# Performance work log

Hardware: AMD Instinct MI355X
Metric: run time of the kernel (lower is better)

## Reference

```python
import jax, jax.numpy as jnp
import numpy as np

B, T, D = 64, 1024, 256   # batch, steps, obs dim
H, L, S = 512, 64, 4      # rnn hidden, latent dim, num_samples
LOG_2PI = float(np.log(2.0 * np.pi))


def setup_inputs() -> dict:
    key = jax.random.key(0)
    ks = jax.random.split(key, 6)
    return {
        "inputs": jax.random.normal(ks[0], (B, T, D), dtype=jnp.float32),
        "noise": jax.random.normal(ks[1], (T, S * B, L), dtype=jnp.float32),
        "W_x": jax.random.normal(ks[2], (D + L, 3 * H), dtype=jnp.float32) * 0.05,
        "W_h": jax.random.normal(ks[3], (H, 3 * H), dtype=jnp.float32) * 0.05,
        "b": jnp.zeros((3 * H,), dtype=jnp.float32),
        "W_d": jax.random.normal(ks[4], (H, 2 * L), dtype=jnp.float32) * 0.05,
        "b_d": jnp.zeros((2 * L,), dtype=jnp.float32),
    }


def _forward(inputs, noise, W_x, W_h, b, W_d, b_d):
    # inputs: [B, T, D]; scan over time with carry (rnn_state h, prev latent z)
    xs_t = jnp.swapaxes(inputs, 0, 1)  # [T, B, D]

    def step(carry, xs):
        h, z_prev = carry              # h: [S*B, H], z_prev: [S*B, L]
        x_t, eps_t = xs                # x_t: [B, D], eps_t: [S*B, L]
        x_tiled = jnp.tile(x_t, (S, 1))            # [S*B, D]
        rnn_in = jnp.concatenate([x_tiled, z_prev], axis=-1)  # [S*B, D+L]
        xg = rnn_in @ W_x + b                      # [S*B, 3H]
        hg_zr = h @ W_h[:, : 2 * H]                # update/reset recurrent part
        z_gate = jax.nn.sigmoid(xg[:, :H] + hg_zr[:, :H])
        r_gate = jax.nn.sigmoid(xg[:, H : 2 * H] + hg_zr[:, H:])
        n_cand = jnp.tanh(xg[:, 2 * H :] + (r_gate * h) @ W_h[:, 2 * H :])
        h_new = (1.0 - z_gate) * n_cand + z_gate * h  # GRU state, rnn_out == h_new
        # posterior dist p(z[t] | h[t]): diag Gaussian
        dp = h_new @ W_d + b_d                     # [S*B, 2L]
        mu, raw = dp[:, :L], dp[:, L:]
        sigma = jax.nn.softplus(raw) + 1e-4
        log_sigma = jnp.log(sigma)
        z = mu + sigma * eps_t                     # reparameterized sample
        ent = jnp.sum(0.5 * (LOG_2PI + 1.0) + log_sigma, axis=-1)          # [S*B]
        lp = jnp.sum(-0.5 * eps_t * eps_t - log_sigma - 0.5 * LOG_2PI, axis=-1)
        return (h_new, z), (z, ent, lp)

    h0 = jnp.zeros((S * B, H), dtype=inputs.dtype)
    z0 = jnp.zeros((S * B, L), dtype=inputs.dtype)
    _, (zs, ents, lps) = jax.lax.scan(step, (h0, z0), (xs_t, noise))
    # zs: [T, S*B, L] -> [S, B, T, L]
    sampled_z = jnp.swapaxes(zs, 0, 1).reshape(S, B, T, L)
    entropies = jnp.swapaxes(ents, 0, 1).reshape(S, B, T)
    log_probs = jnp.swapaxes(lps, 0, 1).reshape(S, B, T)
    return sampled_z, entropies, log_probs


def reference(inputs, noise, W_x, W_h, b, W_d, b_d):
    return _forward(inputs, noise, W_x, W_h, b, W_d, b_d)
```

## Files before the change

kernel.cpp:

```cpp
#include <hip/hip_runtime.h>
#include <stdint.h>


#define NWG  128u

typedef __bf16 bf16;
typedef __attribute__((ext_vector_type(8))) __bf16 bf16x8;
typedef __attribute__((ext_vector_type(8))) short  s16x8;
typedef __attribute__((ext_vector_type(4))) float  f32x4;
typedef __attribute__((ext_vector_type(4))) unsigned int u32x4;
typedef __attribute__((ext_vector_type(2))) unsigned long long u64x2;

__device__ __forceinline__ f32x4 mfma16(bf16x8 a, bf16x8 b, f32x4 c) {
  return __builtin_amdgcn_mfma_f32_16x16x32_bf16(
      __builtin_bit_cast(s16x8, a), __builtin_bit_cast(s16x8, b), c, 0, 0, 0);
}

__global__ void repack_kernel(const float* __restrict__ W_x,
                              const float* __restrict__ W_h,
                              const float* __restrict__ W_d,
                              bf16* __restrict__ Whs, bf16* __restrict__ Wxz,
                              bf16* __restrict__ Wdf, bf16* __restrict__ Wxx)
{
  unsigned e = blockIdx.x*256u + threadIdx.x;
  if (e < 786432u) {
    unsigned c = e/49152u, r0 = e%49152u;
    unsigned kc = r0/3072u, r1 = r0%3072u;
    unsigned q = r1/768u, r2 = r1%768u;
    unsigned n = r2/8u, j = r2%8u;
    unsigned k = kc*32u + q*8u + j;
    unsigned colg = (n>>5)*512u + c*32u + (n&31u);
    Whs[e] = (bf16)W_h[k*1536u + colg];
  } else if (e < 884736u) {
    unsigned e1 = e - 786432u;
    unsigned c = e1/6144u, r0 = e1%6144u;
    unsigned kc = r0/3072u, r1 = r0%3072u;
    unsigned q = r1/768u, r2 = r1%768u;
    unsigned n = r2/8u, j = r2%8u;
    unsigned k = 256u + kc*32u + q*8u + j;
    unsigned colg = (n>>5)*512u + c*32u + (n&31u);
    Wxz[e1] = (bf16)W_x[k*1536u + colg];
  } else if (e < 950272u) {
    unsigned e2 = e - 884736u;
    unsigned kc = e2/4096u, r0 = e2%4096u;
    unsigned q = r0/1024u, r1 = r0%1024u;
    unsigned n = r1/8u, j = r1%8u;
    unsigned k = kc*32u + q*8u + j;
    Wdf[e2] = (bf16)W_d[k*128u + n];
  } else if (e < 1343488u) {
    unsigned e3 = e - 950272u;
    unsigned c = e3/24576u, r0 = e3%24576u;
    unsigned kc = r0/3072u, r1 = r0%3072u;
    unsigned q = r1/768u, r2 = r1%768u;
    unsigned n = r2/8u, j = r2%8u;
    unsigned k = kc*32u + q*8u + j;
    unsigned colg = (n>>5)*512u + c*32u + (n&31u);
    Wxx[e3] = (bf16)W_x[k*1536u + colg];
  }
}

__global__ void xpose_kernel(const float* __restrict__ x, bf16* __restrict__ xT)
{
  unsigned t = blockIdx.x, tid = threadIdx.x;
  unsigned row = tid>>2, seg = tid&3u;
  const float* src = x + ((size_t)row*1024u + t)*256u + seg*64u;
  bf16* dst = xT + (size_t)t*16384u + row*256u + seg*64u;
  #pragma unroll
  for (int i = 0; i < 8; ++i) {
    f32x4 v0 = *(const f32x4*)(src + i*8);
    f32x4 v1 = *(const f32x4*)(src + i*8 + 4);
    bf16x8 o;
    #pragma unroll
    for (int j = 0; j < 4; ++j) { o[j] = (bf16)v0[j]; o[4+j] = (bf16)v1[j]; }
    *(bf16x8*)(dst + i*8) = o;
  }
}

__global__ void __launch_bounds__(256) xgx_kernel(const bf16* __restrict__ xT,
                                                  const bf16* __restrict__ Wxx,
                                                  const float* __restrict__ bias,
                                                  bf16* __restrict__ xgx,
                                                  unsigned t0)
{
  __shared__ bf16 WxS[24576];
  __shared__ bf16 otile[6144];
  unsigned bid = blockIdx.x, lt = bid>>4, c = bid&15u, tid = threadIdx.x;
  unsigned t = t0 + lt;
  { const u32x4* s = (const u32x4*)(Wxx + (size_t)c*24576u); u32x4* d = (u32x4*)WxS;
    #pragma unroll
    for (int i=0;i<12;i++) d[tid+256u*i] = s[tid+256u*i]; }
  __syncthreads();
  unsigned wave = tid>>6, lane = tid&63u, q = lane>>4, m = lane&15u;
  f32x4 zero4 = {0.f,0.f,0.f,0.f};
  f32x4 acc[6];
  #pragma unroll
  for (int nt=0;nt<6;nt++) acc[nt] = zero4;
  const bf16* ap = xT + (size_t)t*16384u + (16u*wave + m)*256u + q*8u;
  #pragma unroll
  for (int kc=0;kc<8;kc++) {
    bf16x8 a = *(const bf16x8*)(ap + kc*32);
    #pragma unroll
    for (int nt=0;nt<6;nt++) {
      bf16x8 bb = *(const bf16x8*)(WxS + (((unsigned)kc*4u+q)*96u + (unsigned)nt*16u + m)*8u);
      acc[nt] = mfma16(a, bb, acc[nt]);
    }
  }
  #pragma unroll
  for (int nt=0;nt<6;nt++) {
    unsigned n = (unsigned)nt*16u + m;
    unsigned colg = (n>>5)*512u + c*32u + (n&31u);
    float bv = bias[colg];
    #pragma unroll
    for (int reg=0;reg<4;reg++)
      otile[(16u*wave + 4u*q + (unsigned)reg)*96u + n] = (bf16)(acc[nt][reg] + bv);
  }
  __syncthreads();
  { u32x4* d = (u32x4*)(xgx + (size_t)(lt*16u + c)*6144u);
    const u32x4* s = (const u32x4*)otile;
    #pragma unroll
    for (int i=0;i<3;i++) d[tid+256u*i] = s[tid+256u*i]; }
}

__device__ __forceinline__ void rb_barrier(unsigned* __restrict__ flags,
                                           unsigned tid, unsigned lane,
                                           unsigned wave, unsigned c,
                                           unsigned target)
{
  __syncthreads();
  if (tid == 0)
    __hip_atomic_store(&flags[c], target, __ATOMIC_RELAXED,
                       __HIP_MEMORY_SCOPE_AGENT);
  if (wave == 0) {
    for (;;) {
      unsigned v = target;
      if (lane < 16u)
        v = __hip_atomic_load(&flags[lane], __ATOMIC_RELAXED,
                              __HIP_MEMORY_SCOPE_AGENT);
      if (__all((int)(v >= target))) break;
      __builtin_amdgcn_s_sleep(1);
    }
  }
  __syncthreads();
}

#define LDS_REC 159744
__global__ void __launch_bounds__(256, 1) rec_kernel(
    const bf16* __restrict__ Whs_g, const bf16* __restrict__ Wxz_g,
    const bf16* __restrict__ Wdf_g, const bf16* __restrict__ xgx,
    const float* __restrict__ noise, const float* __restrict__ b_d,
    float* __restrict__ out, bf16* __restrict__ hbuf, bf16* __restrict__ ubuf,
    bf16* __restrict__ zbuf, unsigned* __restrict__ bar,
    unsigned t0, unsigned tlen)
{
  extern __shared__ char smem[];
  bf16*  WhS  = (bf16*)(smem);
  bf16*  WxzS = (bf16*)(smem + 98304);
  bf16*  hA   = (bf16*)(smem + 110592);
  bf16*  zA   = (bf16*)(smem + 143360);
  bf16*  stg  = (bf16*)(smem + 147456);
  float* zgSf = (float*)(smem + 149504);
  bf16*  muS  = (bf16*)(smem + 147456);
  float* rawS = (float*)(smem + 151552);

  const unsigned tid = threadIdx.x;
  const unsigned wave = tid>>6, lane = tid&63u, q = lane>>4, m = lane&15u;
  const unsigned mt = wave&1u, gt = wave>>1;
  const unsigned r = blockIdx.x>>4, c = blockIdx.x&15u;
  const unsigned b0 = (r&1u)*32u;
  const unsigned rowG0 = r*32u;
  const unsigned zrow = tid>>3, zi = tid&7u;
  unsigned* flags = bar + (size_t)r*64u;

  { const u32x4* s = (const u32x4*)(Whs_g + (size_t)c*49152u); u32x4* d = (u32x4*)WhS;
    #pragma unroll
    for (int i=0;i<24;i++) d[tid+256u*i] = s[tid+256u*i]; }
  { const u32x4* s = (const u32x4*)(Wxz_g + (size_t)c*6144u); u32x4* d = (u32x4*)WxzS;
    #pragma unroll
    for (int i=0;i<3;i++) d[tid+256u*i] = s[tid+256u*i]; }
  bf16x8 wd[16][2];
  #pragma unroll
  for (int kc=0;kc<16;kc++) {
    #pragma unroll
    for (int nw=0;nw<2;nw++)
      wd[kc][nw] = *(const bf16x8*)(Wdf_g +
          ((((unsigned)kc*4u+q)*128u + wave*32u + (unsigned)nw*16u + m)*8u));
  }
  float bd0 = b_d[wave*32u + m], bd1 = b_d[wave*32u + 16u + m];
  float hstate[4];
  if (t0 == 0) {
    u32x4 zz = {0,0,0,0};
    u32x4* d = (u32x4*)hA;
    #pragma unroll
    for (int i=0;i<8;i++) d[tid+256u*i] = zz;
    ((u32x4*)zA)[tid] = zz;
    #pragma unroll
    for (int reg=0;reg<4;reg++) hstate[reg] = 0.f;
    __syncthreads();
  } else {
    const u32x4* s = (const u32x4*)(hbuf + ((size_t)(1u*8u + r)*16u)*1024u);
    u32x4* d = (u32x4*)hA;
    #pragma unroll
    for (int i=0;i<8;i++) d[tid+256u*i] = s[tid+256u*i];
    bf16x8 zv = *(const bf16x8*)(zbuf + ((size_t)(rowG0 + zrow)*64u + zi*8u));
    *(bf16x8*)(zA + ((size_t)zi*32u + zrow)*8u) = zv;
    __syncthreads();
    unsigned cl = gt*16u + m;
    #pragma unroll
    for (int reg=0;reg<4;reg++)
      hstate[reg] = (float)hA[((c*4u + (cl>>3))*32u + 16u*mt + 4u*q + (unsigned)reg)*8u + (cl&7u)];
  }

  const unsigned tend = t0 + tlen;
  for (unsigned t = t0; t < tend; ++t) {
    unsigned par = t & 1u;
    unsigned kb = 2u*(t - t0);
    __bf16 xv1[2][4]; __bf16 xv2[4];
    { size_t base = ((size_t)((t - t0)*16u + c)*64u + b0 + 16u*mt + 4u*q)*96u + m;
      #pragma unroll
      for (int nt=0;nt<2;nt++)
        #pragma unroll
        for (int reg=0;reg<4;reg++)
          xv1[nt][reg] = xgx[base + (unsigned)reg*96u + gt*32u + (unsigned)nt*16u];
      #pragma unroll
      for (int reg=0;reg<4;reg++)
        xv2[reg] = xgx[base + (unsigned)reg*96u + 64u + gt*16u];
    }
    f32x4 eps0, eps1;
    { const float* np = noise + ((size_t)t*256u + rowG0 + zrow)*64u + zi*8u;
      eps0 = *(const f32x4*)np; eps1 = *(const f32x4*)(np + 4); }

    f32x4 accP0 = {0.f,0.f,0.f,0.f}, accP1 = {0.f,0.f,0.f,0.f};
    #pragma unroll
    for (int kc=0;kc<2;kc++) {
      bf16x8 a = *(const bf16x8*)(zA + (((unsigned)kc*4u+q)*32u + 16u*mt + m)*8u);
      accP0 = mfma16(a, *(const bf16x8*)(WxzS + (((unsigned)kc*4u+q)*96u + gt*32u + m)*8u), accP0);
      accP1 = mfma16(a, *(const bf16x8*)(WxzS + (((unsigned)kc*4u+q)*96u + gt*32u + 16u + m)*8u), accP1);
    }
    #pragma unroll
    for (int kc=0;kc<16;kc++) {
      bf16x8 a = *(const bf16x8*)(hA + (((unsigned)kc*4u+q)*32u + 16u*mt + m)*8u);
      accP0 = mfma16(a, *(const bf16x8*)(WhS + (((unsigned)kc*4u+q)*96u + gt*32u + m)*8u), accP0);
      accP1 = mfma16(a, *(const bf16x8*)(WhS + (((unsigned)kc*4u+q)*96u + gt*32u + 16u + m)*8u), accP1);
    }
    #pragma unroll
    for (int reg=0;reg<4;reg++) {
      unsigned rloc = 16u*mt + 4u*q + (unsigned)reg;
      float g0 = accP0[reg] + (float)xv1[0][reg];
      float g1 = accP1[reg] + (float)xv1[1][reg];
      float s0 = 1.f/(1.f + __expf(-g0));
      float s1 = 1.f/(1.f + __expf(-g1));
      if (gt == 0) {
        zgSf[rloc*32u + m]       = s0;
        zgSf[rloc*32u + 16u + m] = s1;
      } else {
        unsigned cl0 = m, cl1 = 16u + m;
        float h0 = (float)hA[((c*4u + (cl0>>3))*32u + rloc)*8u + (cl0&7u)];
        float h1 = (float)hA[((c*4u + (cl1>>3))*32u + rloc)*8u + (cl1&7u)];
        stg[((cl0>>3)*32u + rloc)*8u + (cl0&7u)] = (bf16)(s0*h0);
        stg[((cl1>>3)*32u + rloc)*8u + (cl1&7u)] = (bf16)(s1*h1);
      }
    }
    __syncthreads();
    { size_t blk = ((size_t)(par*8u + r)*16u + c)*1024u;
      unsigned long long v = *(const unsigned long long*)(stg + (size_t)tid*4u);
      __hip_atomic_store((unsigned long long*)(ubuf + blk + (size_t)tid*4u), v,
                         __ATOMIC_RELAXED, __HIP_MEMORY_SCOPE_AGENT); }
    rb_barrier(flags, tid, lane, wave, c, kb + 1u);

    unsigned long long uf0[16], uf1[16];
    { unsigned long long* ub = (unsigned long long*)ubuf;
      size_t b64 = ((size_t)(par*8u + r)*16u)*256u + (q*32u + 16u*mt + m)*2u;
      #pragma unroll
      for (int kc=0;kc<16;kc++) {
        uf0[kc] = __hip_atomic_load(ub + b64 + (unsigned)kc*256u,
                                    __ATOMIC_RELAXED, __HIP_MEMORY_SCOPE_AGENT);
        uf1[kc] = __hip_atomic_load(ub + b64 + (unsigned)kc*256u + 1u,
                                    __ATOMIC_RELAXED, __HIP_MEMORY_SCOPE_AGENT);
      }
    }
    f32x4 accNa = {0.f,0.f,0.f,0.f}, accNb = {0.f,0.f,0.f,0.f};
    #pragma unroll
    for (int kc=0;kc<2;kc++) {
      bf16x8 a = *(const bf16x8*)(zA + (((unsigned)kc*4u+q)*32u + 16u*mt + m)*8u);
      accNa = mfma16(a, *(const bf16x8*)(WxzS + (((unsigned)kc*4u+q)*96u + 64u + gt*16u + m)*8u), accNa);
    }
    #pragma unroll
    for (int kc=0;kc<16;kc++) {
      u64x2 tt; tt[0] = uf0[kc]; tt[1] = uf1[kc];
      bf16x8 a = __builtin_bit_cast(bf16x8, tt);
      f32x4& acc = (kc & 1) ? accNb : accNa;
      acc = mfma16(a, *(const bf16x8*)(WhS + (((unsigned)kc*4u+q)*96u + 64u + gt*16u + m)*8u), acc);
    }
    { unsigned colL2 = gt*16u + m;
      #pragma unroll
      for (int reg=0;reg<4;reg++) {
        unsigned rloc = 16u*mt + 4u*q + (unsigned)reg;
        float zg = zgSf[rloc*32u + colL2];
        float pre = accNa[reg] + accNb[reg] + (float)xv2[reg];
        float e2 = __expf(2.f*pre);
        float nc = 1.f - 2.f/(e2 + 1.f);
        float hn = (1.f - zg)*nc + zg*hstate[reg];
        hstate[reg] = hn;
        stg[((colL2>>3)*32u + rloc)*8u + (colL2&7u)] = (bf16)hn;
      }
    }
    __syncthreads();
    { size_t blk = ((size_t)(par*8u + r)*16u + c)*1024u;
      unsigned long long v = *(const unsigned long long*)(stg + (size_t)tid*4u);
      __hip_atomic_store((unsigned long long*)(hbuf + blk + (size_t)tid*4u), v,
                         __ATOMIC_RELAXED, __HIP_MEMORY_SCOPE_AGENT); }
    rb_barrier(flags, tid, lane, wave, c, kb + 2u);
    { unsigned long long* s = (unsigned long long*)(hbuf + ((size_t)(par*8u + r)*16u)*1024u);
      unsigned long long* d = (unsigned long long*)hA;
      unsigned long long gtmp[16];
      #pragma unroll
      for (int i=0;i<16;i++)
        gtmp[i] = __hip_atomic_load(s + tid + 256u*i,
                                    __ATOMIC_RELAXED, __HIP_MEMORY_SCOPE_AGENT);
      #pragma unroll
      for (int i=0;i<16;i++) d[tid + 256u*i] = gtmp[i];
    }
    __syncthreads();

    f32x4 dp00={0.f,0.f,0.f,0.f}, dp01={0.f,0.f,0.f,0.f};
    f32x4 dp10={0.f,0.f,0.f,0.f}, dp11={0.f,0.f,0.f,0.f};
    #pragma unroll
    for (int kc=0;kc<16;kc++) {
      bf16x8 a0 = *(const bf16x8*)(hA + (((unsigned)kc*4u+q)*32u + m)*8u);
      bf16x8 a1 = *(const bf16x8*)(hA + (((unsigned)kc*4u+q)*32u + 16u + m)*8u);
      dp00 = mfma16(a0, wd[kc][0], dp00);
      dp01 = mfma16(a0, wd[kc][1], dp01);
      dp10 = mfma16(a1, wd[kc][0], dp10);
      dp11 = mfma16(a1, wd[kc][1], dp11);
    }
    if (wave < 2u) {
      #pragma unroll
      for (int reg=0;reg<4;reg++) {
        unsigned r0 = 4u*q + (unsigned)reg;
        muS[r0*64u + wave*32u + m]              = (bf16)(dp00[reg] + bd0);
        muS[r0*64u + wave*32u + 16u + m]        = (bf16)(dp01[reg] + bd1);
        muS[(r0+16u)*64u + wave*32u + m]        = (bf16)(dp10[reg] + bd0);
        muS[(r0+16u)*64u + wave*32u + 16u + m]  = (bf16)(dp11[reg] + bd1);
      }
    } else {
      unsigned cb = (wave - 2u)*32u;
      #pragma unroll
      for (int reg=0;reg<4;reg++) {
        unsigned r0 = 4u*q + (unsigned)reg;
        rawS[r0*64u + cb + m]              = dp00[reg] + bd0;
        rawS[r0*64u + cb + 16u + m]        = dp01[reg] + bd1;
        rawS[(r0+16u)*64u + cb + m]        = dp10[reg] + bd0;
        rawS[(r0+16u)*64u + cb + 16u + m]  = dp11[reg] + bd1;
      }
    }
    __syncthreads();
    {
      bf16x8 mu8 = *(const bf16x8*)(muS + (size_t)zrow*64u + zi*8u);
      f32x4 rw0 = *(const f32x4*)(rawS + (size_t)zrow*64u + zi*8u);
      f32x4 rw1 = *(const f32x4*)(rawS + (size_t)zrow*64u + zi*8u + 4u);
      float ent = 0.f, lp = 0.f;
      float zf[8];
      #pragma unroll
      for (int j=0;j<8;j++) {
        float raw = (j < 4) ? rw0[j] : rw1[j-4];
        float sp = (raw > 20.f) ? raw : __logf(1.f + __expf(raw));
        sp += 1e-4f;
        float ls = __logf(sp);
        float e = (j < 4) ? eps0[j] : eps1[j-4];
        float zv = (float)mu8[j] + sp*e;
        zf[j] = zv;
        ent += ls;
        lp  -= 0.5f*e*e + ls;
      }
      ent += 8.f*1.4189385332046727f;
      lp  -= 8.f*0.9189385332046727f;
      bf16x8 zb;
      #pragma unroll
      for (int j=0;j<8;j++) zb[j] = (bf16)zf[j];
      *(bf16x8*)(zA + ((size_t)zi*32u + zrow)*8u) = zb;
      if ((zrow>>1) == c) {
        float* zo = out + ((size_t)(rowG0 + zrow)*1024u + t)*64u + zi*8u;
        f32x4 o0 = {zf[0],zf[1],zf[2],zf[3]}, o1 = {zf[4],zf[5],zf[6],zf[7]};
        *(f32x4*)zo = o0; *((f32x4*)zo + 1) = o1;
        if (t == tend - 1u)
          *(bf16x8*)(zbuf + ((size_t)(rowG0 + zrow)*64u + zi*8u)) = zb;
      }
      ent += __shfl_down(ent, 4); lp += __shfl_down(lp, 4);
      ent += __shfl_down(ent, 2); lp += __shfl_down(lp, 2);
      ent += __shfl_down(ent, 1); lp += __shfl_down(lp, 1);
      if (zi == 0u && (zrow>>1) == c) {
        out[16777216u + (size_t)(rowG0 + zrow)*1024u + t] = ent;
        out[17039360u + (size_t)(rowG0 + zrow)*1024u + t] = lp;
      }
    }
    __syncthreads();
  }
}

extern "C" void kernel_launch(void* const* d_in, const int* in_sizes, int n_in,
                              void* d_out, int out_size, void* d_ws, size_t ws_size,
                              hipStream_t stream)
{
  const float* x     = (const float*)d_in[0];
  const float* noise = (const float*)d_in[1];
  const float* W_x   = (const float*)d_in[2];
  const float* W_h   = (const float*)d_in[3];
  const float* bias  = (const float*)d_in[4];
  const float* W_d   = (const float*)d_in[5];
  const float* b_d   = (const float*)d_in[6];
  float* out = (float*)d_out;
  char* ws = (char*)d_ws;

  size_t off = 0;
  unsigned* bar = (unsigned*)(ws + off);  off += 32768;
  bf16* Wdf  = (bf16*)(ws + off);         off += 65536ull*2;
  bf16* Whs  = (bf16*)(ws + off);         off += 786432ull*2;
  bf16* Wxz  = (bf16*)(ws + off);         off += 98304ull*2;
  bf16* Wxx  = (bf16*)(ws + off);         off += 393216ull*2;
  bf16* hbuf = (bf16*)(ws + off);         off += 262144ull*2;
  bf16* ubuf = (bf16*)(ws + off);         off += 262144ull*2;
  bf16* zbuf = (bf16*)(ws + off);         off += 16384ull*2;
  bf16* xT   = (bf16*)(ws + off);         off += 16777216ull*2;
  bf16* xgx  = (bf16*)(ws + off);
  size_t fixed = off;

  unsigned tlen = 1024;
  while (tlen > 64 && fixed + (size_t)tlen*196608ull > ws_size) tlen >>= 1;
  unsigned nch = 1024/tlen;

  hipMemsetAsync(bar, 0, 32768, stream);
  repack_kernel<<<5248, 256, 0, stream>>>(W_x, W_h, W_d, Whs, Wxz, Wdf, Wxx);
  xpose_kernel<<<1024, 256, 0, stream>>>(x, xT);
  hipFuncSetAttribute((const void*)rec_kernel,
                      hipFuncAttributeMaxDynamicSharedMemorySize, LDS_REC);
  for (unsigned ch = 0; ch < nch; ++ch) {
    unsigned t0 = ch*tlen;
    xgx_kernel<<<tlen*16, 256, 0, stream>>>(xT, Wxx, bias, xgx, t0);
    rec_kernel<<<NWG, 256, LDS_REC, stream>>>(Whs, Wxz, Wdf, xgx, noise, b_d,
                                              out, hbuf, ubuf, zbuf,
                                              bar + (size_t)ch*512u, t0, tlen);
  }
}
```

Measured before the change: 9.236 ms.

## Remap workgroups so row groups share an XCD and sync through L2

After: 9.011 ms. -2.4%, faster.

```diff
diff --git a/kernel.cpp b/kernel.cpp
--- a/kernel.cpp
+++ b/kernel.cpp
@@ -14,6 +14,22 @@
 __device__ __forceinline__ f32x4 mfma16(bf16x8 a, bf16x8 b, f32x4 c) {
   return __builtin_amdgcn_mfma_f32_16x16x32_bf16(
       __builtin_bit_cast(s16x8, a), __builtin_bit_cast(s16x8, b), c, 0, 0, 0);
+}
+
+__device__ __forceinline__ unsigned ld_u32_sc0(const unsigned* p) {
+  unsigned v;
+  asm volatile("global_load_dword %0, %1, off sc0\n\ts_waitcnt vmcnt(0)"
+               : "=v"(v) : "v"(p) : "memory");
+  return v;
+}
+__device__ __forceinline__ u32x4 ld_u128_sc0(const void* p) {
+  u32x4 v;
+  asm volatile("global_load_dwordx4 %0, %1, off sc0" : "=v"(v) : "v"(p));
+  return v;
+}
+__device__ __forceinline__ void vm_wait0() {
+  asm volatile("s_waitcnt vmcnt(0)" ::: "memory");
+  __builtin_amdgcn_sched_barrier(0);
 }
 
 __global__ void repack_kernel(const float* __restrict__ W_x,
@@ -121,7 +137,7 @@
     for (int i=0;i<3;i++) d[tid+256u*i] = s[tid+256u*i]; }
 }
 
-__device__ __forceinline__ void rb_barrier(unsigned* __restrict__ flags,
+__device__ __forceinline__ void rb_bar_llc(unsigned* __restrict__ flags,
                                            unsigned tid, unsigned lane,
                                            unsigned wave, unsigned c,
                                            unsigned target)
@@ -142,6 +158,24 @@
   }
   __syncthreads();
 }
+__device__ __forceinline__ void rb_bar_l2(unsigned* __restrict__ flags,
+                                          unsigned tid, unsigned lane,
+                                          unsigned wave, unsigned c,
+                                          unsigned target)
+{
+  __syncthreads();
+  if (tid == 0)
+    __hip_atomic_store(&flags[c], target, __ATOMIC_RELAXED,
+                       __HIP_MEMORY_SCOPE_WORKGROUP);
+  if (wave == 0) {
+    for (;;) {
+      unsigned v = target;
+      if (lane < 16u) v = ld_u32_sc0(&flags[lane]);
+      if (__all((int)(v >= target))) break;
+    }
+  }
+  __syncthreads();
+}
 
 #define LDS_REC 159744
 __global__ void __launch_bounds__(256, 1) rec_kernel(
@@ -165,11 +199,11 @@
   const unsigned tid = threadIdx.x;
   const unsigned wave = tid>>6, lane = tid&63u, q = lane>>4, m = lane&15u;
   const unsigned mt = wave&1u, gt = wave>>1;
-  const unsigned r = blockIdx.x>>4, c = blockIdx.x&15u;
+  const unsigned r = blockIdx.x & 7u, c = blockIdx.x >> 3;
   const unsigned b0 = (r&1u)*32u;
   const unsigned rowG0 = r*32u;
   const unsigned zrow = tid>>3, zi = tid&7u;
-  unsigned* flags = bar + (size_t)r*64u;
+  unsigned* rb = bar + (size_t)r*512u;
 
   { const u32x4* s = (const u32x4*)(Whs_g + (size_t)c*49152u); u32x4* d = (u32x4*)WhS;
     #pragma unroll
@@ -186,6 +220,55 @@
           ((((unsigned)kc*4u+q)*128u + wave*32u + (unsigned)nw*16u + m)*8u));
   }
   float bd0 = b_d[wave*32u + m], bd1 = b_d[wave*32u + 16u + m];
+
+  bool l2m;
+  {
+    unsigned* ts = rb + 128u;
+    unsigned myxcd;
+    asm volatile("s_getreg_b32 %0, hwreg(HW_REG_XCC_ID)" : "=s"(myxcd));
+    myxcd = (myxcd & 15u) + 1u;
+    if (tid == 0)
+      __hip_atomic_store(&rb[32u + c], myxcd, __ATOMIC_RELAXED,
+                         __HIP_MEMORY_SCOPE_AGENT);
+    rb_bar_llc(rb, tid, lane, wave, c, 1u);
+    bool xcdok;
+    { unsigned v = myxcd;
+      if (lane < 16u)
+        v = __hip_atomic_load(&rb[32u + lane], __ATOMIC_RELAXED,
+                              __HIP_MEMORY_SCOPE_AGENT);
+      xcdok = (bool)__all((int)(v == myxcd));
+    }
+    if (tid < 16u)
+      __hip_atomic_store(&ts[c*16u + tid], 0xA0000000u + (c<<8) + tid,
+                         __ATOMIC_RELAXED, __HIP_MEMORY_SCOPE_WORKGROUP);
+    rb_bar_llc(rb, tid, lane, wave, c, 2u);
+    unsigned jj = tid>>4, ii = tid&15u;
+    bool okA = (ld_u32_sc0(&ts[tid]) == 0xA0000000u + (jj<<8) + ii);
+    rb_bar_llc(rb, tid, lane, wave, c, 3u);
+    if (tid < 16u)
+      __hip_atomic_store(&ts[c*16u + tid], 0xB0000000u + (c<<8) + tid,
+                         __ATOMIC_RELAXED, __HIP_MEMORY_SCOPE_WORKGROUP);
+    rb_bar_llc(rb, tid, lane, wave, c, 4u);
+    bool okB = (ld_u32_sc0(&ts[tid]) == 0xB0000000u + (jj<<8) + ii);
+    unsigned* sc = (unsigned*)stg;
+    sc[0] = 1u; __syncthreads();
+    if (!(okA && okB)) sc[0] = 0u;
+    __syncthreads();
+    unsigned myok = (sc[0] != 0u) ? 1u : 2u;
+    __syncthreads();
+    if (tid == 0)
+      __hip_atomic_store(&rb[96u + c], myok, __ATOMIC_RELAXED,
+                         __HIP_MEMORY_SCOPE_AGENT);
+    rb_bar_llc(rb, tid, lane, wave, c, 5u);
+    { unsigned v = 1u;
+      if (lane < 16u)
+        v = __hip_atomic_load(&rb[96u + lane], __ATOMIC_RELAXED,
+                              __HIP_MEMORY_SCOPE_AGENT);
+      l2m = xcdok && (bool)__all((int)(v == 1u));
+    }
+  }
+  unsigned* l2f = rb + 64u;
+
   float hstate[4];
   if (t0 == 0) {
     u32x4 zz = {0,0,0,0};
@@ -263,19 +346,36 @@
     __syncthreads();
     { size_t blk = ((size_t)(par*8u + r)*16u + c)*1024u;
       unsigned long long v = *(const unsigned long long*)(stg + (size_t)tid*4u);
-      __hip_atomic_store((unsigned long long*)(ubuf + blk + (size_t)tid*4u), v,
-                         __ATOMIC_RELAXED, __HIP_MEMORY_SCOPE_AGENT); }
-    rb_barrier(flags, tid, lane, wave, c, kb + 1u);
-
-    unsigned long long uf0[16], uf1[16];
-    { unsigned long long* ub = (unsigned long long*)ubuf;
+      if (l2m)
+        __hip_atomic_store((unsigned long long*)(ubuf + blk + (size_t)tid*4u), v,
+                           __ATOMIC_RELAXED, __HIP_MEMORY_SCOPE_WORKGROUP);
+      else
+        __hip_atomic_store((unsigned long long*)(ubuf + blk + (size_t)tid*4u), v,
+                           __ATOMIC_RELAXED, __HIP_MEMORY_SCOPE_AGENT); }
+    if (l2m) rb_bar_l2 (l2f, tid, lane, wave, c, kb + 1u);
+    else     rb_bar_llc(rb,  tid, lane, wave, c, kb + 6u);
+
+    bf16x8 ufr[16];
+    if (l2m) {
+      const char* ub = (const char*)ubuf + (size_t)(par*8u + r)*32768u
+                       + (q*32u + 16u*mt + m)*16u;
+      u32x4 tmp[16];
+      #pragma unroll
+      for (int kc=0;kc<16;kc++) tmp[kc] = ld_u128_sc0(ub + kc*2048);
+      vm_wait0();
+      #pragma unroll
+      for (int kc=0;kc<16;kc++) ufr[kc] = __builtin_bit_cast(bf16x8, tmp[kc]);
+    } else {
+      unsigned long long* ubp = (unsigned long long*)ubuf;
       size_t b64 = ((size_t)(par*8u + r)*16u)*256u + (q*32u + 16u*mt + m)*2u;
       #pragma unroll
       for (int kc=0;kc<16;kc++) {
-        uf0[kc] = __hip_atomic_load(ub + b64 + (unsigned)kc*256u,
+        unsigned long long a0 = __hip_atomic_load(ubp + b64 + (unsigned)kc*256u,
                                     __ATOMIC_RELAXED, __HIP_MEMORY_SCOPE_AGENT);
-        uf1[kc] = __hip_atomic_load(ub + b64 + (unsigned)kc*256u + 1u,
+        unsigned long long a1 = __hip_atomic_load(ubp + b64 + (unsigned)kc*256u + 1u,
                                     __ATOMIC_RELAXED, __HIP_MEMORY_SCOPE_AGENT);
+        u64x2 tt; tt[0] = a0; tt[1] = a1;
+        ufr[kc] = __builtin_bit_cast(bf16x8, tt);
       }
     }
     f32x4 accNa = {0.f,0.f,0.f,0.f}, accNb = {0.f,0.f,0.f,0.f};
@@ -286,10 +386,8 @@
     }
     #pragma unroll
     for (int kc=0;kc<16;kc++) {
-      u64x2 tt; tt[0] = uf0[kc]; tt[1] = uf1[kc];
-      bf16x8 a = __builtin_bit_cast(bf16x8, tt);
       f32x4& acc = (kc & 1) ? accNb : accNa;
-      acc = mfma16(a, *(const bf16x8*)(WhS + (((unsigned)kc*4u+q)*96u + 64u + gt*16u + m)*8u), acc);
+      acc = mfma16(ufr[kc], *(const bf16x8*)(WhS + (((unsigned)kc*4u+q)*96u + 64u + gt*16u + m)*8u), acc);
     }
     { unsigned colL2 = gt*16u + m;
       #pragma unroll
@@ -307,10 +405,25 @@
     __syncthreads();
     { size_t blk = ((size_t)(par*8u + r)*16u + c)*1024u;
       unsigned long long v = *(const unsigned long long*)(stg + (size_t)tid*4u);
-      __hip_atomic_store((unsigned long long*)(hbuf + blk + (size_t)tid*4u), v,
-                         __ATOMIC_RELAXED, __HIP_MEMORY_SCOPE_AGENT); }
-    rb_barrier(flags, tid, lane, wave, c, kb + 2u);
-    { unsigned long long* s = (unsigned long long*)(hbuf + ((size_t)(par*8u + r)*16u)*1024u);
+      if (l2m)
+        __hip_atomic_store((unsigned long long*)(hbuf + blk + (size_t)tid*4u), v,
+                           __ATOMIC_RELAXED, __HIP_MEMORY_SCOPE_WORKGROUP);
+      else
+        __hip_atomic_store((unsigned long long*)(hbuf + blk + (size_t)tid*4u), v,
+                           __ATOMIC_RELAXED, __HIP_MEMORY_SCOPE_AGENT); }
+    if (l2m) rb_bar_l2 (l2f, tid, lane, wave, c, kb + 2u);
+    else     rb_bar_llc(rb,  tid, lane, wave, c, kb + 7u);
+    if (l2m) {
+      const char* hb = (const char*)hbuf + (size_t)(par*8u + r)*32768u
+                       + (size_t)tid*16u;
+      u32x4 g[8];
+      #pragma unroll
+      for (int i=0;i<8;i++) g[i] = ld_u128_sc0(hb + i*4096);
+      vm_wait0();
+      #pragma unroll
+      for (int i=0;i<8;i++) ((u32x4*)hA)[tid + 256u*i] = g[i];
+    } else {
+      unsigned long long* s = (unsigned long long*)(hbuf + ((size_t)(par*8u + r)*16u)*1024u);
       unsigned long long* d = (unsigned long long*)hA;
       unsigned long long gtmp[16];
       #pragma unroll
@@ -412,7 +525,7 @@
   char* ws = (char*)d_ws;
 
   size_t off = 0;
-  unsigned* bar = (unsigned*)(ws + off);  off += 32768;
+  unsigned* bar = (unsigned*)(ws + off);  off += 262144;
   bf16* Wdf  = (bf16*)(ws + off);         off += 65536ull*2;
   bf16* Whs  = (bf16*)(ws + off);         off += 786432ull*2;
   bf16* Wxz  = (bf16*)(ws + off);         off += 98304ull*2;
@@ -428,7 +541,7 @@
   while (tlen > 64 && fixed + (size_t)tlen*196608ull > ws_size) tlen >>= 1;
   unsigned nch = 1024/tlen;
 
-  hipMemsetAsync(bar, 0, 32768, stream);
+  hipMemsetAsync(bar, 0, 262144, stream);
   repack_kernel<<<5248, 256, 0, stream>>>(W_x, W_h, W_d, Whs, Wxz, Wdf, Wxx);
   xpose_kernel<<<1024, 256, 0, stream>>>(x, xT);
   hipFuncSetAttribute((const void*)rec_kernel,
@@ -438,6 +551,6 @@
     xgx_kernel<<<tlen*16, 256, 0, stream>>>(xT, Wxx, bias, xgx, t0);
     rec_kernel<<<NWG, 256, LDS_REC, stream>>>(Whs, Wxz, Wdf, xgx, noise, b_d,
                                               out, hbuf, ubuf, zbuf,
-                                              bar + (size_t)ch*512u, t0, tlen);
-  }
-}
+                                              bar + (size_t)ch*4096u, t0, tlen);
+  }
+}
```
